# Optimization experiments

Hardware: AMD Instinct MI355X
Metric: run time of the kernel (lower is better)

The kernel has to match this reference:

```python
import jax, jax.numpy as jnp
import numpy as np

B, S, H, I, E, K = 2, 512, 1024, 4096, 8, 2
LN_EPS = 1e-5


def setup_inputs() -> dict:
    key = jax.random.key(0)
    ks = jax.random.split(key, 5)
    sc = 0.02  # init scale for weights
    return {
        "hidden_states": jax.random.normal(ks[0], (B, S, H), jnp.float32),
        "ln_w": jnp.ones((H,), jnp.float32),
        "ln_b": jnp.zeros((H,), jnp.float32),
        "Wr": jax.random.normal(ks[1], (E, H), jnp.float32) * sc,  # router [out=E, in=H]
        "br": jnp.zeros((E,), jnp.float32),
        "W1": jax.random.normal(ks[2], (E, I, H), jnp.float32) * sc,  # dense1 per expert [out=I, in=H]
        "b1": jnp.zeros((E, I), jnp.float32),
        "W2": jax.random.normal(ks[3], (E, H, I), jnp.float32) * sc,  # dense2 per expert [out=H, in=I]
        "b2": jnp.zeros((E, H), jnp.float32),
    }


def reference(hidden_states, ln_w, ln_b, Wr, br, W1, b1, W2, b2):
    # Eval mode: no jitter noise, no dropout.
    residual = hidden_states
    mu = jnp.mean(hidden_states, axis=-1, keepdims=True)
    var = jnp.mean(jnp.square(hidden_states - mu), axis=-1, keepdims=True)
    x = (hidden_states - mu) * jax.lax.rsqrt(var + LN_EPS) * ln_w + ln_b  # [B,S,H]

    logits = jnp.einsum("bsh,eh->bse", x, Wr) + br  # [B,S,E]
    topw, topi = jax.lax.top_k(logits, K)  # [B,S,K]
    topw = jax.nn.softmax(topw, axis=-1)
    # Combine weights per expert (top-k indices are distinct, so scatter == first-match)
    combine = jnp.sum(jax.nn.one_hot(topi, E, dtype=x.dtype) * topw[..., None], axis=-2)  # [B,S,E]

    # Dense per-expert FFN (reference form of gather-FFN-scatter); combine zeros out unselected experts
    a = jax.nn.gelu(jnp.einsum("bsh,eih->bsei", x, W1) + b1, approximate=False)  # [B,S,E,I]
    y = jnp.einsum("bsei,ehi->bseh", a, W2) + b2  # [B,S,E,H]
    out = residual + jnp.einsum("bse,bseh->bsh", combine, y)

    probs = jax.nn.softmax(logits, axis=-1)
    usage = jnp.mean(probs, axis=(0, 1))  # [E]
    balance_loss = E * jnp.sum(usage * usage) - 1.0
    return out, balance_loss
```

## Files before the change

### kernel.cpp

```cpp
#include <hip/hip_runtime.h>
#include <hip/hip_bf16.h>
#include <math.h>
#include <stdint.h>

#define T_TOK 1024
#define H_DIM 1024
#define I_DIM 4096
#define E_NUM 8
#define NSLOT (2 * T_TOK)
#define WELEM 33554432

typedef __attribute__((ext_vector_type(8))) short bf16x8;
typedef __attribute__((ext_vector_type(4))) float f32x4;

#define MFMA_BF16(a, b, c) __builtin_amdgcn_mfma_f32_16x16x32_bf16(a, b, c, 0, 0, 0)

__device__ __forceinline__ short f2bf(float f) {
  union { float f; unsigned u; } x; x.f = f;
  unsigned r = (x.u + 0x7fffu + ((x.u >> 16) & 1u)) >> 16;
  return (short)r;
}
__device__ __forceinline__ int pack2bf(float a, float b) {
  return ((int)(unsigned short)f2bf(a)) | (((int)f2bf(b)) << 16);
}

typedef __attribute__((address_space(3))) unsigned int as3_u32;
typedef const __attribute__((address_space(1))) unsigned int as1_u32c;
__device__ __forceinline__ void glds16(const void* g, void* l) {
  __builtin_amdgcn_global_load_lds((as1_u32c*)g, (as3_u32*)l, 16, 0, 0);
}

union BBCast { int4 i4; bf16x8 v; };

__global__ __launch_bounds__(256) void k_ln_router(
    const float* __restrict__ x, const float* __restrict__ ln_w,
    const float* __restrict__ ln_b, const float* __restrict__ Wr,
    const float* __restrict__ br,
    short* __restrict__ xln, int* __restrict__ sel_e, float* __restrict__ sel_w,
    float* __restrict__ probs, float* __restrict__ out) {
  const int t = blockIdx.x;
  const int tid = threadIdx.x;
  const int lane = tid & 63, wid = tid >> 6;
  __shared__ float sx[H_DIM];
  __shared__ float redS[8];
  __shared__ float slog[E_NUM];

  float4 v = ((const float4*)(x + (size_t)t * H_DIM))[tid];
  ((float4*)(out + (size_t)t * H_DIM))[tid] = v;
  float s = v.x + v.y + v.z + v.w;
  float ss = v.x * v.x + v.y * v.y + v.z * v.z + v.w * v.w;
  for (int o = 32; o > 0; o >>= 1) { s += __shfl_down(s, o); ss += __shfl_down(ss, o); }
  if (lane == 0) { redS[wid] = s; redS[4 + wid] = ss; }
  __syncthreads();
  float st = redS[0] + redS[1] + redS[2] + redS[3];
  float sst = redS[4] + redS[5] + redS[6] + redS[7];
  float mu = st * (1.0f / H_DIM);
  float var = sst * (1.0f / H_DIM) - mu * mu;
  float rs = rsqrtf(var + 1e-5f);

  float4 lw = ((const float4*)ln_w)[tid];
  float4 lb = ((const float4*)ln_b)[tid];
  float4 xn;
  xn.x = (v.x - mu) * rs * lw.x + lb.x;
  xn.y = (v.y - mu) * rs * lw.y + lb.y;
  xn.z = (v.z - mu) * rs * lw.z + lb.z;
  xn.w = (v.w - mu) * rs * lw.w + lb.w;
  sx[4 * tid + 0] = xn.x; sx[4 * tid + 1] = xn.y;
  sx[4 * tid + 2] = xn.z; sx[4 * tid + 3] = xn.w;
  short4 s4;
  s4.x = f2bf(xn.x); s4.y = f2bf(xn.y); s4.z = f2bf(xn.z); s4.w = f2bf(xn.w);
  ((short4*)(xln + (size_t)t * H_DIM))[tid] = s4;
  __syncthreads();

  for (int e = 2 * wid; e < 2 * wid + 2; ++e) {
    float p = 0.f;
    for (int h = lane; h < H_DIM; h += 64) p += sx[h] * Wr[e * H_DIM + h];
    for (int o = 32; o > 0; o >>= 1) p += __shfl_down(p, o);
    if (lane == 0) slog[e] = p + br[e];
  }
  __syncthreads();

  if (tid == 0) {
    float lg[E_NUM];
    for (int e = 0; e < E_NUM; ++e) lg[e] = slog[e];
    int i0 = 0;
    for (int e = 1; e < E_NUM; ++e) if (lg[e] > lg[i0]) i0 = e;
    int i1 = (i0 == 0) ? 1 : 0;
    for (int e = 0; e < E_NUM; ++e) if (e != i0 && lg[e] > lg[i1]) i1 = e;
    float w1e = __expf(lg[i1] - lg[i0]);
    float den = 1.f + w1e;
    sel_e[2 * t] = i0; sel_w[2 * t] = 1.f / den;
    sel_e[2 * t + 1] = i1; sel_w[2 * t + 1] = w1e / den;
    float se = 0.f, pe[E_NUM];
    for (int e = 0; e < E_NUM; ++e) { pe[e] = __expf(lg[e] - lg[i0]); se += pe[e]; }
    float inv = 1.f / se;
    for (int e = 0; e < E_NUM; ++e) probs[t * E_NUM + e] = pe[e] * inv;
  }
}

__global__ __launch_bounds__(512) void k_route(
    const int* __restrict__ sel_e, const float* __restrict__ sel_w,
    const float* __restrict__ probs,
    int* __restrict__ counts, int* __restrict__ basep,
    int* __restrict__ tlist, int* __restrict__ sel_idx,
    float* __restrict__ wslot, float* __restrict__ loss_out) {
  const int wid = threadIdx.x >> 6;
  const int lane = threadIdx.x & 63;
  __shared__ int scnt[E_NUM];
  __shared__ float susage[E_NUM];

  int cnt = 0;
  for (int s0 = 0; s0 < NSLOT; s0 += 64) {
    int s = s0 + lane;
    bool m = (sel_e[s] == wid);
    unsigned long long mk = __ballot(m);
    int pre = __popcll(mk & ((1ULL << lane) - 1ULL));
    if (m) {
      int idx = cnt + pre;
      sel_idx[s] = idx;
      tlist[wid * T_TOK + idx] = s >> 1;
      wslot[wid * T_TOK + idx] = sel_w[s];
    }
    cnt += __popcll(mk);
  }
  if (lane == 0) scnt[wid] = cnt;

  float u = 0.f;
  for (int t = lane; t < T_TOK; t += 64) u += probs[t * E_NUM + wid];
  for (int o = 32; o > 0; o >>= 1) u += __shfl_down(u, o);
  if (lane == 0) susage[wid] = u * (1.0f / T_TOK);
  __syncthreads();

  if (threadIdx.x == 0) {
    int b = 0;
    for (int e = 0; e < E_NUM; ++e) { basep[e] = b; counts[e] = scnt[e]; b += scnt[e]; }
    float sq = 0.f;
    for (int e = 0; e < E_NUM; ++e) sq += susage[e] * susage[e];
    *loss_out = (float)E_NUM * sq - 1.0f;
  }
}

__global__ __launch_bounds__(256) void k_cvt(const float* __restrict__ src,
                                             short* __restrict__ dst, int n) {
  const int stride = gridDim.x * blockDim.x;
  for (int i = blockIdx.x * blockDim.x + threadIdx.x; i < (n >> 3); i += stride) {
    float4 a = ((const float4*)src)[2 * i];
    float4 b = ((const float4*)src)[2 * i + 1];
    int4 p;
    p.x = pack2bf(a.x, a.y); p.y = pack2bf(a.z, a.w);
    p.z = pack2bf(b.x, b.y); p.w = pack2bf(b.z, b.w);
    ((int4*)dst)[i] = p;
  }
}

__global__ __launch_bounds__(256) void k_ffn1(
    const short* __restrict__ xln, const short* __restrict__ W1b,
    const float* __restrict__ b1, const int* __restrict__ counts,
    const int* __restrict__ basep, const int* __restrict__ tlist,
    short* __restrict__ a_buf) {
  const int e = blockIdx.z;
  const int cnt = counts[e];
  const int m0 = blockIdx.y * 128;
  if (m0 >= cnt) return;
  const int n0 = blockIdx.x * 128;

  __shared__ __align__(16) short As[2][128 * 32];
  __shared__ __align__(16) short Bs[2][128 * 32];

  const int tid = threadIdx.x;
  const int lane = tid & 63, wid = tid >> 6;
  const int wr = wid >> 1, wc = wid & 1;
  const int fr = lane & 15, fq = lane >> 4;

  int r0 = m0 + (tid >> 2); if (r0 >= cnt) r0 = cnt - 1;
  int r1 = m0 + 64 + (tid >> 2); if (r1 >= cnt) r1 = cnt - 1;
  const short* ag0 = xln + (size_t)tlist[e * T_TOK + r0] * H_DIM + (tid & 3) * 8;
  const short* ag1 = xln + (size_t)tlist[e * T_TOK + r1] * H_DIM + (tid & 3) * 8;
  const short* bg0 = W1b + ((size_t)e * I_DIM + n0 + (tid >> 2)) * H_DIM + (tid & 3) * 8;
  const short* bg1 = bg0 + (size_t)64 * H_DIM;

  f32x4 acc[4][4];
#pragma unroll
  for (int i = 0; i < 4; ++i)
#pragma unroll
    for (int j = 0; j < 4; ++j) acc[i][j] = (f32x4)0.f;

#define STAGE(kk, buf)                                  \
  {                                                     \
    glds16(ag0 + (kk), &As[buf][tid * 8]);              \
    glds16(ag1 + (kk), &As[buf][(256 + tid) * 8]);      \
    glds16(bg0 + (kk), &Bs[buf][tid * 8]);              \
    glds16(bg1 + (kk), &Bs[buf][(256 + tid) * 8]);      \
  }

  STAGE(0, 0);
  __syncthreads();

  int cur = 0;
  for (int kt = 0; kt < H_DIM / 32; ++kt) {
    if (kt + 1 < H_DIM / 32) STAGE((kt + 1) * 32, cur ^ 1);
    bf16x8 af[4], bb[4];
#pragma unroll
    for (int mi = 0; mi < 4; ++mi)
      af[mi] = *(const bf16x8*)&As[cur][(wr * 64 + mi * 16 + fr) * 32 + fq * 8];
#pragma unroll
    for (int ni = 0; ni < 4; ++ni)
      bb[ni] = *(const bf16x8*)&Bs[cur][(wc * 64 + ni * 16 + fr) * 32 + fq * 8];
#pragma unroll
    for (int mi = 0; mi < 4; ++mi)
#pragma unroll
      for (int ni = 0; ni < 4; ++ni)
        acc[mi][ni] = MFMA_BF16(af[mi], bb[ni], acc[mi][ni]);
    __syncthreads();
    cur ^= 1;
  }
#undef STAGE

  const int slot0 = basep[e] + m0;
  float b1v[4];
#pragma unroll
  for (int ni = 0; ni < 4; ++ni)
    b1v[ni] = b1[e * I_DIM + n0 + wc * 64 + ni * 16 + fr];
#pragma unroll
  for (int mi = 0; mi < 4; ++mi)
#pragma unroll
    for (int j = 0; j < 4; ++j) {
      int r = wr * 64 + mi * 16 + fq * 4 + j;
      if (m0 + r < cnt) {
        size_t rowoff = (size_t)(slot0 + r) * I_DIM;
#pragma unroll
        for (int ni = 0; ni < 4; ++ni) {
          int colg = n0 + wc * 64 + ni * 16 + fr;
          float vv = acc[mi][ni][j] + b1v[ni];
          float g = 0.5f * vv * (1.0f + erff(vv * 0.70710678118654752f));
          a_buf[rowoff + colg] = f2bf(g);
        }
      }
    }
}

__global__ __launch_bounds__(256) void k_ffn2(
    const short* __restrict__ a_buf, const short* __restrict__ W2b,
    const float* __restrict__ b2, const int* __restrict__ counts,
    const int* __restrict__ basep, const int* __restrict__ tlist,
    const float* __restrict__ wslot, float* __restrict__ out) {
  const int z = blockIdx.z;
  const int e = z >> 2;
  const int kc = z & 3;
  const int CH = I_DIM / 4;
  const int cnt = counts[e];
  const int m0 = blockIdx.y * 128;
  if (m0 >= cnt) return;
  const int n0 = blockIdx.x * 128;

  __shared__ __align__(16) short As[2][128 * 32];
  __shared__ __align__(16) short Bs[2][128 * 32];

  const int tid = threadIdx.x;
  const int lane = tid & 63, wid = tid >> 6;
  const int wr = wid >> 1, wc = wid & 1;
  const int fr = lane & 15, fq = lane >> 4;

  int r0 = m0 + (tid >> 2); if (r0 >= cnt) r0 = cnt - 1;
  int r1 = m0 + 64 + (tid >> 2); if (r1 >= cnt) r1 = cnt - 1;
  const int sb = basep[e];
  const short* ag0 = a_buf + (size_t)(sb + r0) * I_DIM + kc * CH + (tid & 3) * 8;
  const short* ag1 = a_buf + (size_t)(sb + r1) * I_DIM + kc * CH + (tid & 3) * 8;
  const short* bg0 = W2b + ((size_t)e * H_DIM + n0 + (tid >> 2)) * I_DIM + kc * CH + (tid & 3) * 8;
  const short* bg1 = bg0 + (size_t)64 * I_DIM;

  f32x4 acc[4][4];
#pragma unroll
  for (int i = 0; i < 4; ++i)
#pragma unroll
    for (int j = 0; j < 4; ++j) acc[i][j] = (f32x4)0.f;

#define STAGE(kk, buf)                                  \
  {                                                     \
    glds16(ag0 + (kk), &As[buf][tid * 8]);              \
    glds16(ag1 + (kk), &As[buf][(256 + tid) * 8]);      \
    glds16(bg0 + (kk), &Bs[buf][tid * 8]);              \
    glds16(bg1 + (kk), &Bs[buf][(256 + tid) * 8]);      \
  }

  STAGE(0, 0);
  __syncthreads();

  const int KT = CH / 32;
  int cur = 0;
  for (int kt = 0; kt < KT; ++kt) {
    if (kt + 1 < KT) STAGE((kt + 1) * 32, cur ^ 1);
    bf16x8 af[4], bb[4];
#pragma unroll
    for (int mi = 0; mi < 4; ++mi)
      af[mi] = *(const bf16x8*)&As[cur][(wr * 64 + mi * 16 + fr) * 32 + fq * 8];
#pragma unroll
    for (int ni = 0; ni < 4; ++ni)
      bb[ni] = *(const bf16x8*)&Bs[cur][(wc * 64 + ni * 16 + fr) * 32 + fq * 8];
#pragma unroll
    for (int mi = 0; mi < 4; ++mi)
#pragma unroll
      for (int ni = 0; ni < 4; ++ni)
        acc[mi][ni] = MFMA_BF16(af[mi], bb[ni], acc[mi][ni]);
    __syncthreads();
    cur ^= 1;
  }
#undef STAGE

  float b2v[4];
#pragma unroll
  for (int ni = 0; ni < 4; ++ni)
    b2v[ni] = 0.25f * b2[e * H_DIM + n0 + wc * 64 + ni * 16 + fr];
#pragma unroll
  for (int mi = 0; mi < 4; ++mi)
#pragma unroll
    for (int j = 0; j < 4; ++j) {
      int r = wr * 64 + mi * 16 + fq * 4 + j;
      if (m0 + r < cnt) {
        int tok = tlist[e * T_TOK + m0 + r];
        float w = wslot[e * T_TOK + m0 + r];
        float* orow = out + (size_t)tok * H_DIM;
#pragma unroll
        for (int ni = 0; ni < 4; ++ni) {
          int colg = n0 + wc * 64 + ni * 16 + fr;
          atomicAdd(&orow[colg], w * (acc[mi][ni][j] + b2v[ni]));
        }
      }
    }
}

__global__ __launch_bounds__(256) void k_ffn1_f32(
    const short* __restrict__ xln, const float* __restrict__ W1,
    const float* __restrict__ b1, const int* __restrict__ counts,
    const int* __restrict__ basep, const int* __restrict__ tlist,
    short* __restrict__ a_buf) {
  const int e = blockIdx.z;
  const int cnt = counts[e];
  const int m0 = blockIdx.y * 128;
  if (m0 >= cnt) return;
  const int n0 = blockIdx.x * 128;
  __shared__ __align__(16) short As[2][128 * 32];
  __shared__ __align__(16) float Bsf[2][128 * 32];
  const int tid = threadIdx.x;
  const int lane = tid & 63, wid = tid >> 6;
  const int wr = wid >> 1, wc = wid & 1;
  const int fr = lane & 15, fq = lane >> 4;
  int r0 = m0 + (tid >> 2); if (r0 >= cnt) r0 = cnt - 1;
  int r1 = m0 + 64 + (tid >> 2); if (r1 >= cnt) r1 = cnt - 1;
  const short* ag0 = xln + (size_t)tlist[e * T_TOK + r0] * H_DIM + (tid & 3) * 8;
  const short* ag1 = xln + (size_t)tlist[e * T_TOK + r1] * H_DIM + (tid & 3) * 8;
  const int bro = tid >> 3;
  const int bslot = (tid & 7) ^ (bro & 7);
  const float* bg = W1 + ((size_t)e * I_DIM + n0 + bro) * H_DIM + bslot * 4;
  f32x4 acc[4][4];
#pragma unroll
  for (int i = 0; i < 4; ++i)
#pragma unroll
    for (int j = 0; j < 4; ++j) acc[i][j] = (f32x4)0.f;
#define STAGE(kk, buf)                                                      \
  {                                                                         \
    glds16(ag0 + (kk), &As[buf][tid * 8]);                                  \
    glds16(ag1 + (kk), &As[buf][(256 + tid) * 8]);                          \
    _Pragma("unroll") for (int i = 0; i < 4; ++i)                           \
        glds16(bg + (size_t)(i * 32) * H_DIM + (kk),                        \
               &Bsf[buf][(i * 256 + tid) * 4]);                             \
  }
  STAGE(0, 0);
  __syncthreads();
  int cur = 0;
  for (int kt = 0; kt < H_DIM / 32; ++kt) {
    if (kt + 1 < H_DIM / 32) STAGE((kt + 1) * 32, cur ^ 1);
    bf16x8 af[4], bb[4];
#pragma unroll
    for (int mi = 0; mi < 4; ++mi)
      af[mi] = *(const bf16x8*)&As[cur][(wr * 64 + mi * 16 + fr) * 32 + fq * 8];
#pragma unroll
    for (int ni = 0; ni < 4; ++ni) {
      const int row = wc * 64 + ni * 16 + fr;
      const int base = row * 128 + fq * 32;
      const int sw = (row & 7) << 4;
      f32x4 lo = *(const f32x4*)((const char*)&Bsf[cur][0] + (base ^ sw));
      f32x4 hi = *(const f32x4*)((const char*)&Bsf[cur][0] + ((base + 16) ^ sw));
      BBCast c;
      c.i4.x = pack2bf(lo[0], lo[1]); c.i4.y = pack2bf(lo[2], lo[3]);
      c.i4.z = pack2bf(hi[0], hi[1]); c.i4.w = pack2bf(hi[2], hi[3]);
      bb[ni] = c.v;
    }
#pragma unroll
    for (int mi = 0; mi < 4; ++mi)
#pragma unroll
      for (int ni = 0; ni < 4; ++ni)
        acc[mi][ni] = MFMA_BF16(af[mi], bb[ni], acc[mi][ni]);
    __syncthreads();
    cur ^= 1;
  }
#undef STAGE
  const int slot0 = basep[e] + m0;
  float b1v[4];
#pragma unroll
  for (int ni = 0; ni < 4; ++ni)
    b1v[ni] = b1[e * I_DIM + n0 + wc * 64 + ni * 16 + fr];
#pragma unroll
  for (int mi = 0; mi < 4; ++mi)
#pragma unroll
    for (int j = 0; j < 4; ++j) {
      int r = wr * 64 + mi * 16 + fq * 4 + j;
      if (m0 + r < cnt) {
        size_t rowoff = (size_t)(slot0 + r) * I_DIM;
#pragma unroll
        for (int ni = 0; ni < 4; ++ni) {
          int colg = n0 + wc * 64 + ni * 16 + fr;
          float vv = acc[mi][ni][j] + b1v[ni];
          float g = 0.5f * vv * (1.0f + erff(vv * 0.70710678118654752f));
          a_buf[rowoff + colg] = f2bf(g);
        }
      }
    }
}

__global__ __launch_bounds__(256) void k_ffn2_f32(
    const short* __restrict__ a_buf, const float* __restrict__ W2,
    const float* __restrict__ b2, const int* __restrict__ counts,
    const int* __restrict__ basep, const int* __restrict__ tlist,
    const float* __restrict__ wslot, float* __restrict__ out, int lg) {
  const int z = blockIdx.z;
  const int e = z >> lg;
  const int kc = z & ((1 << lg) - 1);
  const int CH = I_DIM >> lg;
  const int cnt = counts[e];
  const int m0 = blockIdx.y * 128;
  if (m0 >= cnt) return;
  const int n0 = blockIdx.x * 128;
  __shared__ __align__(16) short As[2][128 * 32];
  __shared__ __align__(16) float Bsf[2][128 * 32];
  const int tid = threadIdx.x;
  const int lane = tid & 63, wid = tid >> 6;
  const int wr = wid >> 1, wc = wid & 1;
  const int fr = lane & 15, fq = lane >> 4;
  int r0 = m0 + (tid >> 2); if (r0 >= cnt) r0 = cnt - 1;
  int r1 = m0 + 64 + (tid >> 2); if (r1 >= cnt) r1 = cnt - 1;
  const int sb = basep[e];
  const short* ag0 = a_buf + (size_t)(sb + r0) * I_DIM + kc * CH + (tid & 3) * 8;
  const short* ag1 = a_buf + (size_t)(sb + r1) * I_DIM + kc * CH + (tid & 3) * 8;
  const int bro = tid >> 3;
  const int bslot = (tid & 7) ^ (bro & 7);
  const float* bg = W2 + ((size_t)e * H_DIM + n0 + bro) * I_DIM + kc * CH + bslot * 4;
  f32x4 acc[4][4];
#pragma unroll
  for (int i = 0; i < 4; ++i)
#pragma unroll
    for (int j = 0; j < 4; ++j) acc[i][j] = (f32x4)0.f;
#define STAGE(kk, buf)                                                      \
  {                                                                         \
    glds16(ag0 + (kk), &As[buf][tid * 8]);                                  \
    glds16(ag1 + (kk), &As[buf][(256 + tid) * 8]);                          \
    _Pragma("unroll") for (int i = 0; i < 4; ++i)                           \
        glds16(bg + (size_t)(i * 32) * I_DIM + (kk),                        \
               &Bsf[buf][(i * 256 + tid) * 4]);                             \
  }
  STAGE(0, 0);
  __syncthreads();
  const int KT = CH / 32;
  int cur = 0;
  for (int kt = 0; kt < KT; ++kt) {
    if (kt + 1 < KT) STAGE((kt + 1) * 32, cur ^ 1);
    bf16x8 af[4], bb[4];
#pragma unroll
    for (int mi = 0; mi < 4; ++mi)
      af[mi] = *(const bf16x8*)&As[cur][(wr * 64 + mi * 16 + fr) * 32 + fq * 8];
#pragma unroll
    for (int ni = 0; ni < 4; ++ni) {
      const int row = wc * 64 + ni * 16 + fr;
      const int base = row * 128 + fq * 32;
      const int sw = (row & 7) << 4;
      f32x4 lo = *(const f32x4*)((const char*)&Bsf[cur][0] + (base ^ sw));
      f32x4 hi = *(const f32x4*)((const char*)&Bsf[cur][0] + ((base + 16) ^ sw));
      BBCast c;
      c.i4.x = pack2bf(lo[0], lo[1]); c.i4.y = pack2bf(lo[2], lo[3]);
      c.i4.z = pack2bf(hi[0], hi[1]); c.i4.w = pack2bf(hi[2], hi[3]);
      bb[ni] = c.v;
    }
#pragma unroll
    for (int mi = 0; mi < 4; ++mi)
#pragma unroll
      for (int ni = 0; ni < 4; ++ni)
        acc[mi][ni] = MFMA_BF16(af[mi], bb[ni], acc[mi][ni]);
    __syncthreads();
    cur ^= 1;
  }
#undef STAGE
  const float inv = 1.0f / (float)(1 << lg);
  float b2v[4];
#pragma unroll
  for (int ni = 0; ni < 4; ++ni)
    b2v[ni] = inv * b2[e * H_DIM + n0 + wc * 64 + ni * 16 + fr];
#pragma unroll
  for (int mi = 0; mi < 4; ++mi)
#pragma unroll
    for (int j = 0; j < 4; ++j) {
      int r = wr * 64 + mi * 16 + fq * 4 + j;
      if (m0 + r < cnt) {
        int tok = tlist[e * T_TOK + m0 + r];
        float w = wslot[e * T_TOK + m0 + r];
        float* orow = out + (size_t)tok * H_DIM;
#pragma unroll
        for (int ni = 0; ni < 4; ++ni) {
          int colg = n0 + wc * 64 + ni * 16 + fr;
          atomicAdd(&orow[colg], w * (acc[mi][ni][j] + b2v[ni]));
        }
      }
    }
}

extern "C" void kernel_launch(void* const* d_in, const int* in_sizes, int n_in,
                              void* d_out, int out_size, void* d_ws, size_t ws_size,
                              hipStream_t stream) {
  const float* hidden = (const float*)d_in[0];
  const float* ln_w = (const float*)d_in[1];
  const float* ln_b = (const float*)d_in[2];
  const float* Wr = (const float*)d_in[3];
  const float* br = (const float*)d_in[4];
  const float* W1 = (const float*)d_in[5];
  const float* b1 = (const float*)d_in[6];
  const float* W2 = (const float*)d_in[7];
  const float* b2 = (const float*)d_in[8];
  float* out = (float*)d_out;

  char* w = (char*)d_ws;
  int* counts = (int*)(w + 0);
  int* basep = (int*)(w + 256);
  float* probs = (float*)(w + 512);
  int* tlist = (int*)(w + 33280);
  int* sel_e = (int*)(w + 66048);
  int* sel_idx = (int*)(w + 74240);
  float* sel_w = (float*)(w + 82432);
  float* wslot = (float*)(w + 90624);
  short* xln = (short*)(w + 131072);
  short* a_buf = (short*)(w + 2228224);
  short* w_bf = (short*)(w + 19005440);
  const size_t REQ_NEW = 19005440 + (size_t)WELEM * 2;

  k_ln_router<<<T_TOK, 256, 0, stream>>>(hidden, ln_w, ln_b, Wr, br, xln,
                                         sel_e, sel_w, probs, out);
  k_route<<<1, 512, 0, stream>>>(sel_e, sel_w, probs, counts, basep, tlist,
                                 sel_idx, wslot, out + (size_t)T_TOK * H_DIM);

  if (ws_size >= REQ_NEW) {
    k_cvt<<<2048, 256, 0, stream>>>(W1, w_bf, WELEM);
    k_ffn1<<<dim3(I_DIM / 128, T_TOK / 128, E_NUM), 256, 0, stream>>>(
        xln, w_bf, b1, counts, basep, tlist, a_buf);
    k_cvt<<<2048, 256, 0, stream>>>(W2, w_bf, WELEM);
    k_ffn2<<<dim3(H_DIM / 128, T_TOK / 128, E_NUM * 4), 256, 0, stream>>>(
        a_buf, w_bf, b2, counts, basep, tlist, wslot, out);
  } else {
    const int lg = 2;
    k_ffn1_f32<<<dim3(I_DIM / 128, T_TOK / 128, E_NUM), 256, 0, stream>>>(
        xln, W1, b1, counts, basep, tlist, a_buf);
    k_ffn2_f32<<<dim3(H_DIM / 128, T_TOK / 128, E_NUM << lg), 256, 0, stream>>>(
        a_buf, W2, b2, counts, basep, tlist, wslot, out, lg);
  }
}
```

Baseline: 232.8 us.

## Triple-buffer LDS tiles in expert FFN GEMMs with one barrier per step

Both expert GEMM kernels move from two LDS buffers to three and prefetch two k-tiles ahead. A single barrier per iteration now follows a partial vmcnt wait that allows the newest stage's four loads to stay in flight, replacing the two __syncthreads per step. The goal is to hide global-to-LDS load latency and cut synchronization. In exchange, LDS use per block rises from 32KB to 48KB, which may lower occupancy, and correctness depends on the vmcnt count matching the number of async loads issued per stage.

Result: slower. 249.4 us (+7.1%).

```diff
diff --git a/kernel.cpp b/kernel.cpp
--- a/kernel.cpp
+++ b/kernel.cpp
@@ -164,8 +164,8 @@
   if (m0 >= cnt) return;
   const int n0 = blockIdx.x * 128;
 
-  __shared__ __align__(16) short As[2][128 * 32];
-  __shared__ __align__(16) short Bs[2][128 * 32];
+  __shared__ __align__(16) short As[3][128 * 32];
+  __shared__ __align__(16) short Bs[3][128 * 32];
 
   const int tid = threadIdx.x;
   const int lane = tid & 63, wid = tid >> 6;
@@ -194,25 +194,30 @@
   }
 
   STAGE(0, 0);
-  __syncthreads();
-
-  int cur = 0;
-  for (int kt = 0; kt < H_DIM / 32; ++kt) {
-    if (kt + 1 < H_DIM / 32) STAGE((kt + 1) * 32, cur ^ 1);
+  STAGE(32, 1);
+
+  const int KT = H_DIM / 32;
+  for (int kt = 0; kt < KT; ++kt) {
+    if (kt == KT - 1) {
+      asm volatile("s_waitcnt vmcnt(0)" ::: "memory");
+    } else {
+      asm volatile("s_waitcnt vmcnt(4)" ::: "memory");
+    }
+    __builtin_amdgcn_s_barrier();
+    if (kt + 2 < KT) STAGE((kt + 2) * 32, (kt + 2) % 3);
+    const int cb = kt % 3;
     bf16x8 af[4], bb[4];
 #pragma unroll
     for (int mi = 0; mi < 4; ++mi)
-      af[mi] = *(const bf16x8*)&As[cur][(wr * 64 + mi * 16 + fr) * 32 + fq * 8];
+      af[mi] = *(const bf16x8*)&As[cb][(wr * 64 + mi * 16 + fr) * 32 + fq * 8];
 #pragma unroll
     for (int ni = 0; ni < 4; ++ni)
-      bb[ni] = *(const bf16x8*)&Bs[cur][(wc * 64 + ni * 16 + fr) * 32 + fq * 8];
+      bb[ni] = *(const bf16x8*)&Bs[cb][(wc * 64 + ni * 16 + fr) * 32 + fq * 8];
 #pragma unroll
     for (int mi = 0; mi < 4; ++mi)
 #pragma unroll
       for (int ni = 0; ni < 4; ++ni)
         acc[mi][ni] = MFMA_BF16(af[mi], bb[ni], acc[mi][ni]);
-    __syncthreads();
-    cur ^= 1;
   }
 #undef STAGE
 
@@ -253,8 +258,8 @@
   if (m0 >= cnt) return;
   const int n0 = blockIdx.x * 128;
 
-  __shared__ __align__(16) short As[2][128 * 32];
-  __shared__ __align__(16) short Bs[2][128 * 32];
+  __shared__ __align__(16) short As[3][128 * 32];
+  __shared__ __align__(16) short Bs[3][128 * 32];
 
   const int tid = threadIdx.x;
   const int lane = tid & 63, wid = tid >> 6;
@@ -284,26 +289,30 @@
   }
 
   STAGE(0, 0);
-  __syncthreads();
+  STAGE(32, 1);
 
   const int KT = CH / 32;
-  int cur = 0;
   for (int kt = 0; kt < KT; ++kt) {
-    if (kt + 1 < KT) STAGE((kt + 1) * 32, cur ^ 1);
+    if (kt == KT - 1) {
+      asm volatile("s_waitcnt vmcnt(0)" ::: "memory");
+    } else {
+      asm volatile("s_waitcnt vmcnt(4)" ::: "memory");
+    }
+    __builtin_amdgcn_s_barrier();
+    if (kt + 2 < KT) STAGE((kt + 2) * 32, (kt + 2) % 3);
+    const int cb = kt % 3;
     bf16x8 af[4], bb[4];
 #pragma unroll
     for (int mi = 0; mi < 4; ++mi)
-      af[mi] = *(const bf16x8*)&As[cur][(wr * 64 + mi * 16 + fr) * 32 + fq * 8];
+      af[mi] = *(const bf16x8*)&As[cb][(wr * 64 + mi * 16 + fr) * 32 + fq * 8];
 #pragma unroll
     for (int ni = 0; ni < 4; ++ni)
-      bb[ni] = *(const bf16x8*)&Bs[cur][(wc * 64 + ni * 16 + fr) * 32 + fq * 8];
+      bb[ni] = *(const bf16x8*)&Bs[cb][(wc * 64 + ni * 16 + fr) * 32 + fq * 8];
 #pragma unroll
     for (int mi = 0; mi < 4; ++mi)
 #pragma unroll
       for (int ni = 0; ni < 4; ++ni)
         acc[mi][ni] = MFMA_BF16(af[mi], bb[ni], acc[mi][ni]);
-    __syncthreads();
-    cur ^= 1;
   }
 #undef STAGE
 
```
